# Kernel tuning notes

Hardware: AMD Instinct MI355X
Metric: run time of the kernel (lower is better)

Reference implementation:

```python
import jax, jax.numpy as jnp
import numpy as np

N, DIM, DK, DV = 8192, 1024, 128, 128


def setup_inputs() -> dict:
    key = jax.random.key(0)
    ks = jax.random.split(key, 5)
    # Match equinox Linear init scale roughly (uniform(-1/sqrt(in), 1/sqrt(in)))
    lim = 1.0 / np.sqrt(DIM)
    return {
        "x": jax.random.normal(ks[0], (N, DIM), dtype=jnp.float32),
        "Wqk": jax.random.uniform(ks[1], (DK, DIM), jnp.float32, -lim, lim),
        "bqk": jax.random.uniform(ks[2], (DK,), jnp.float32, -lim, lim),
        "Wv": jax.random.uniform(ks[3], (DV, DIM), jnp.float32, -lim, lim),
        "bv": jax.random.uniform(ks[4], (DV,), jnp.float32, -lim, lim),
    }


def reference(x, Wqk, bqk, Wv, bv):
    # shared QK projection: q == k == x @ Wqk^T + bqk  -> [n, dk]
    qk = jnp.einsum("nd,kd->nk", x, Wqk) + bqk
    v = jnp.einsum("nd,vd->nv", x, Wv) + bv  # [n, dv]
    # full n x n score matrix (no 1/sqrt(dk) scaling in the original)
    score = jnp.einsum("ik,jk->ij", qk, qk)  # [n, n]
    score = jax.nn.softmax(score, axis=-1)
    return jnp.einsum("ij,jv->iv", score, v)  # [n, dv]
```

## Files before the change

kernel.cpp:

```cpp
#include <hip/hip_runtime.h>
#include <math.h>

#define NROWS 8192
#define DIMX  1024
#define DKV   128
#define KSPLIT 4
#define KEYS_PER_SPLIT (NROWS / KSPLIT)
#define BN 64
#define QK_SCALE 1.2011224087864498f
#define M_FIX 96.0f

typedef __attribute__((ext_vector_type(8))) short bf16x8;
typedef __attribute__((ext_vector_type(4))) short s16x4;
typedef __attribute__((ext_vector_type(4))) float f32x4;

static __device__ __forceinline__ short f2bf(float f) {
    union { float f; unsigned u; } v; v.f = f;
    unsigned r = v.u + 0x7fff + ((v.u >> 16) & 1);
    return (short)(r >> 16);
}

__global__ __launch_bounds__(256) void wcvt_kernel(
    const float* __restrict__ Wqk, const float* __restrict__ bqk,
    const float* __restrict__ Wv,  const float* __restrict__ bv,
    short* __restrict__ wb, float* __restrict__ bb)
{
    const int idx = blockIdx.x * 1024 + threadIdx.x * 4;
    const bool isqk = idx < DKV * DIMX;
    const float* src = isqk ? (Wqk + idx) : (Wv + (idx - DKV * DIMX));
    const float sc = isqk ? QK_SCALE : 1.0f;
    const float4 f = *(const float4*)src;
    s16x4 o;
    o.x = f2bf(f.x * sc); o.y = f2bf(f.y * sc);
    o.z = f2bf(f.z * sc); o.w = f2bf(f.w * sc);
    *(s16x4*)&wb[idx] = o;
    if (blockIdx.x == 0) {
        const int t = threadIdx.x;
        bb[t] = (t < DKV) ? bqk[t] * QK_SCALE : bv[t - DKV];
    }
}

__global__ __launch_bounds__(256) void proj_kernel(
    const float* __restrict__ x, const short* __restrict__ wb,
    const float* __restrict__ bb, short* __restrict__ qkb, short* __restrict__ vtb)
{
    __shared__ __align__(16) short xb[32 * 1024];

    const int tid  = threadIdx.x;
    const int lane = tid & 63;
    const int wave = tid >> 6;
    const int l15  = lane & 15;
    const int quad = lane >> 4;
    const int mat  = blockIdx.y;
    const int rbase = blockIdx.x * 32;
    const int wr = wave >> 1, wc = wave & 1;
    const short* wsrc = wb + (size_t)mat * DKV * DIMX;

    #pragma unroll 8
    for (int i = 0; i < 32; ++i) {
        const float4 f = *(const float4*)(x + (size_t)(rbase + i) * DIMX + tid * 4);
        s16x4 o;
        o.x = f2bf(f.x); o.y = f2bf(f.y); o.z = f2bf(f.z); o.w = f2bf(f.w);
        *(s16x4*)&xb[i * 1024 + ((tid * 4) ^ ((i & 7) << 3))] = o;
    }
    __syncthreads();

    f32x4 acc[4];
    for (int i = 0; i < 4; ++i) acc[i] = (f32x4)0.0f;

    const int arow = wr * 16 + l15;
    const int aswz = (arow & 7) << 3;
    const short* arowp = &xb[arow * 1024];

    const short* wcol[4];
    for (int nt = 0; nt < 4; ++nt)
        wcol[nt] = wsrc + (size_t)(wc * 64 + nt * 16 + l15) * DIMX + quad * 8;

    bf16x8 bA[4], bB[4];
    for (int nt = 0; nt < 4; ++nt) bA[nt] = *(const bf16x8*)(wcol[nt]);

    for (int kk = 0; kk < 32; kk += 2) {
        for (int nt = 0; nt < 4; ++nt)
            bB[nt] = *(const bf16x8*)(wcol[nt] + (kk + 1) * 32);
        const bf16x8 a0 = *(const bf16x8*)&arowp[(kk * 32 + quad * 8) ^ aswz];
        for (int nt = 0; nt < 4; ++nt)
            acc[nt] = __builtin_amdgcn_mfma_f32_16x16x32_bf16(a0, bA[nt], acc[nt], 0, 0, 0);
        if (kk + 2 < 32)
            for (int nt = 0; nt < 4; ++nt)
                bA[nt] = *(const bf16x8*)(wcol[nt] + (kk + 2) * 32);
        const bf16x8 a1 = *(const bf16x8*)&arowp[((kk + 1) * 32 + quad * 8) ^ aswz];
        for (int nt = 0; nt < 4; ++nt)
            acc[nt] = __builtin_amdgcn_mfma_f32_16x16x32_bf16(a1, bB[nt], acc[nt], 0, 0, 0);
    }

    const int rw = rbase + wr * 16 + quad * 4;
    for (int nt = 0; nt < 4; ++nt) {
        const int col = wc * 64 + nt * 16 + l15;
        const float bias = bb[mat * DKV + col];
        if (mat == 0) {
            for (int r = 0; r < 4; ++r)
                qkb[(size_t)(rw + r) * DKV + col] = f2bf(acc[nt][r] + bias);
        } else {
            s16x4 o;
            o.x = f2bf(acc[nt][0] + bias); o.y = f2bf(acc[nt][1] + bias);
            o.z = f2bf(acc[nt][2] + bias); o.w = f2bf(acc[nt][3] + bias);
            *(s16x4*)&vtb[(size_t)col * NROWS + rw] = o;
        }
    }
}

__global__ __launch_bounds__(256, 2) void flash_kernel(
    const short* __restrict__ qkb, const short* __restrict__ vtb,
    float* __restrict__ opart, float* __restrict__ lpart)
{
    __shared__ __align__(16) short kt[2][64 * 128];
    __shared__ __align__(16) short pb[4][32 * 64];

    const int tid  = threadIdx.x;
    const int lane = tid & 63;
    const int wave = tid >> 6;
    const int l15  = lane & 15;
    const int quad = lane >> 4;
    const int rg   = wave >> 1;
    const int kh   = wave & 1;
    const int rbase = blockIdx.x * 64 + rg * 32;
    const int ks = blockIdx.y;

    unsigned koff[4];
    for (int i = 0; i < 4; ++i) {
        const int krow = wave * 16 + i * 4 + quad;
        koff[i] = (unsigned)krow * 256u
                + (((unsigned)l15 * 16u) ^ (((unsigned)krow & 7u) << 4));
    }

#define FL_ISSUE(buf, j0) do { \
        const char* kb_ = (const char*)qkb + (size_t)(j0) * (DKV * 2); \
        for (int i = 0; i < 4; ++i) \
            __builtin_amdgcn_global_load_lds( \
                (const __attribute__((address_space(1))) void*)(kb_ + koff[i]), \
                (__attribute__((address_space(3))) void*)((char*)&kt[buf][0] + (wave * 4 + i) * 1024), \
                16, 0, 0); \
    } while (0)

    const short* vpb = vtb + (size_t)l15 * NROWS + kh * 32 + quad * 8;
#define LOADV(dst, j0) do { \
        for (int nt_ = 0; nt_ < 8; ++nt_) \
            dst[nt_] = *(const bf16x8*)(vpb + (size_t)nt_ * (16 * NROWS) + (j0)); \
    } while (0)

    bf16x8 qf[2][4];
    #pragma unroll 2
    for (int h = 0; h < 2; ++h) {
        const short* qrow = qkb + (size_t)(rbase + h * 16 + l15) * DKV;
        for (int k = 0; k < 4; ++k)
            qf[h][k] = *(const bf16x8*)(qrow + k * 32 + quad * 8);
    }

    bf16x8 ones;
    for (int j = 0; j < 8; ++j) ones[j] = (short)0x3F80;

    f32x4 oacc[2][8];
    #pragma unroll 2
    for (int h = 0; h < 2; ++h)
        for (int i = 0; i < 8; ++i) oacc[h][i] = (f32x4)0.0f;
    f32x4 lsum[2] = {(f32x4)0.0f, (f32x4)0.0f};

    short* pw = &pb[wave][0];

    const int krow0 = kh * 32 + 2 * l15;
    const int swk0  = ((krow0 & 7) << 3);
    const int pxw = (quad & 1) << 6;
    const int pxr = (l15 & 4) << 4;

#define TILE(CUR, NXT, VC, VN, j0, more) do { \
        if (more) { FL_ISSUE(NXT, (j0) + BN); LOADV(VN, (j0) + BN); } \
        f32x4 s[2][2]; \
        __builtin_amdgcn_s_setprio(1); \
        for (int ntl = 0; ntl < 2; ++ntl) { \
            f32x4 a0 = (f32x4)0.0f, a1 = (f32x4)0.0f; \
            const int rowb = (krow0 + ntl) * 128; \
            const int swk  = swk0 + ntl * 8; \
            for (int k_ = 0; k_ < 4; ++k_) { \
                const bf16x8 b = *(const bf16x8*) \
                    &kt[CUR][rowb + ((k_ * 32 + quad * 8) ^ swk)]; \
                a0 = __builtin_amdgcn_mfma_f32_16x16x32_bf16(qf[0][k_], b, a0, 0, 0, 0); \
                a1 = __builtin_amdgcn_mfma_f32_16x16x32_bf16(qf[1][k_], b, a1, 0, 0, 0); \
            } \
            s[0][ntl] = a0; s[1][ntl] = a1; \
        } \
        __builtin_amdgcn_s_setprio(0); \
        for (int h = 0; h < 2; ++h) \
            for (int ntl = 0; ntl < 2; ++ntl) \
                for (int r = 0; r < 4; ++r) \
                    s[h][ntl][r] = __builtin_amdgcn_exp2f(s[h][ntl][r] - M_FIX); \
        for (int h = 0; h < 2; ++h) \
            for (int r = 0; r < 4; ++r) { \
                const int row = h * 16 + quad * 4 + r; \
                unsigned pk; \
                asm("v_cvt_pk_bf16_f32 %0, %1, %2" : "=v"(pk) : "v"(s[h][0][r]), "v"(s[h][1][r])); \
                *(unsigned*)((char*)pw + row * 128 + ((l15 * 4) ^ pxw)) = pk; \
            } \
        __builtin_amdgcn_s_setprio(1); \
        { \
            const bf16x8 a0 = *(const bf16x8*)((char*)pw + l15 * 128 + ((quad * 16) ^ pxr)); \
            const bf16x8 a1 = *(const bf16x8*)((char*)pw + (16 + l15) * 128 + ((quad * 16) ^ pxr)); \
            lsum[0] = __builtin_amdgcn_mfma_f32_16x16x32_bf16(a0, ones, lsum[0], 0, 0, 0); \
            lsum[1] = __builtin_amdgcn_mfma_f32_16x16x32_bf16(a1, ones, lsum[1], 0, 0, 0); \
            for (int nt_ = 0; nt_ < 8; ++nt_) { \
                oacc[0][nt_] = __builtin_amdgcn_mfma_f32_16x16x32_bf16(a0, VC[nt_], oacc[0][nt_], 0, 0, 0); \
                oacc[1][nt_] = __builtin_amdgcn_mfma_f32_16x16x32_bf16(a1, VC[nt_], oacc[1][nt_], 0, 0, 0); \
            } \
        } \
        __builtin_amdgcn_s_setprio(0); \
        __syncthreads();    \
    } while (0)

    const int j_begin = ks * KEYS_PER_SPLIT;
    const int j_end   = j_begin + KEYS_PER_SPLIT;

    bf16x8 vfA[8], vfB[8];
    FL_ISSUE(0, j_begin);
    LOADV(vfA, j_begin);
    __syncthreads();

    for (int j0 = j_begin; j0 < j_end; j0 += 2 * BN) {
        TILE(0, 1, vfA, vfB, j0, true);
        TILE(1, 0, vfB, vfA, j0 + BN, (j0 + 2 * BN) < j_end);
    }

    float* obuf = (float*)&kt[0][0] + rg * 32 * 128;
    float* lbuf = (float*)&pb[0][0];
    if (kh == 1) {
        #pragma unroll 2
        for (int h = 0; h < 2; ++h) {
            for (int nt = 0; nt < 8; ++nt)
                for (int r = 0; r < 4; ++r)
                    obuf[(h * 16 + quad * 4 + r) * 128 + nt * 16 + l15] = oacc[h][nt][r];
            if (l15 == 0)
                for (int r = 0; r < 4; ++r)
                    lbuf[rg * 32 + h * 16 + quad * 4 + r] = lsum[h][r];
        }
    }
    __syncthreads();
    if (kh == 0) {
        #pragma unroll 2
        for (int h = 0; h < 2; ++h) {
            const int rw = rbase + h * 16 + quad * 4;
            for (int nt = 0; nt < 8; ++nt) {
                const int col = nt * 16 + l15;
                for (int r = 0; r < 4; ++r)
                    opart[((size_t)ks * NROWS + rw + r) * DKV + col] =
                        oacc[h][nt][r] + obuf[(h * 16 + quad * 4 + r) * 128 + col];
            }
            if (l15 == 0)
                for (int r = 0; r < 4; ++r)
                    lpart[ks * NROWS + rw + r] =
                        lsum[h][r] + lbuf[rg * 32 + h * 16 + quad * 4 + r];
        }
    }
#undef FL_ISSUE
#undef LOADV
#undef TILE
}

__global__ __launch_bounds__(256) void combine_kernel(
    const float* __restrict__ opart, const float* __restrict__ lpart,
    float* __restrict__ out)
{
    const int idx = blockIdx.x * 256 + threadIdx.x;
    const int row = idx >> 7;
    float L = 0.f, acc = 0.f;
    for (int s = 0; s < KSPLIT; ++s) {
        L   += lpart[s * NROWS + row];
        acc += opart[(size_t)s * NROWS * DKV + idx];
    }
    out[idx] = acc / L;
}

extern "C" void kernel_launch(void* const* d_in, const int* in_sizes, int n_in,
                              void* d_out, int out_size, void* d_ws, size_t ws_size,
                              hipStream_t stream) {
    const float* x   = (const float*)d_in[0];
    const float* Wqk = (const float*)d_in[1];
    const float* bqk = (const float*)d_in[2];
    const float* Wv  = (const float*)d_in[3];
    const float* bv  = (const float*)d_in[4];
    float* out = (float*)d_out;

    char* ws = (char*)d_ws;
    short* qkb   = (short*)ws;
    short* vtb   = (short*)(ws + (2u << 20));
    short* wb    = (short*)(ws + (4u << 20));
    float* bb    = (float*)(ws + (4u << 20) + (512u << 10));
    float* opart = (float*)(ws + (5u << 20));
    float* lpart = (float*)(ws + (21u << 20));

    wcvt_kernel<<<dim3(256), 256, 0, stream>>>(Wqk, bqk, Wv, bv, wb, bb);
    proj_kernel<<<dim3(256, 2), 256, 0, stream>>>(x, wb, bb, qkb, vtb);
    flash_kernel<<<dim3(NROWS / 64, KSPLIT), 256, 0, stream>>>(qkb, vtb, opart, lpart);
    combine_kernel<<<dim3(NROWS * DKV / 256), 256, 0, stream>>>(opart, lpart, out);
}
```

Measured before the change: 191.0 us.

## Keep P in registers via transposed QK MFMA and stage V through LDS

The score MFMA now takes K as the A operand and Q as B, so its output is transposed and can be packed straight into the A operand of the PV MFMA. This removes the per-tile round trip of P through LDS. K rows are permuted at load time so the register layout lines up. V tiles are now prefetched into double-buffered, swizzled LDS with async global_load_lds instead of direct register loads, which frees VGPRs. The cost is more LDS traffic for V reads and a more complex row permutation that must stay correct.

```diff
diff --git a/kernel.cpp b/kernel.cpp
--- a/kernel.cpp
+++ b/kernel.cpp
@@ -13,6 +13,7 @@
 typedef __attribute__((ext_vector_type(8))) short bf16x8;
 typedef __attribute__((ext_vector_type(4))) short s16x4;
 typedef __attribute__((ext_vector_type(4))) float f32x4;
+typedef __attribute__((ext_vector_type(4))) unsigned u32x4;
 
 static __device__ __forceinline__ short f2bf(float f) {
     union { float f; unsigned u; } v; v.f = f;
@@ -114,7 +115,7 @@
     float* __restrict__ opart, float* __restrict__ lpart)
 {
     __shared__ __align__(16) short kt[2][64 * 128];
-    __shared__ __align__(16) short pb[4][32 * 64];
+    __shared__ __align__(16) short vt[2][128 * 64];
 
     const int tid  = threadIdx.x;
     const int lane = tid & 63;
@@ -125,27 +126,33 @@
     const int kh   = wave & 1;
     const int rbase = blockIdx.x * 64 + rg * 32;
     const int ks = blockIdx.y;
-
-    unsigned koff[4];
+    const int swzr = (l15 & 7) << 3;
+
+    unsigned koff[4], voff[4];
     for (int i = 0; i < 4; ++i) {
         const int krow = wave * 16 + i * 4 + quad;
-        koff[i] = (unsigned)krow * 256u
+        const int s = krow & 7;
+        const int srow = (krow & ~7) | (((s & 1) << 2) | (s >> 1));
+        koff[i] = (unsigned)srow * 256u
                 + (((unsigned)l15 * 16u) ^ (((unsigned)krow & 7u) << 4));
+        const int vrow = wave * 32 + i * 8 + (lane >> 3);
+        voff[i] = (unsigned)vrow * (unsigned)(NROWS * 2)
+                + ((((unsigned)lane & 7u) * 16u) ^ (((unsigned)vrow & 7u) << 4));
     }
 
 #define FL_ISSUE(buf, j0) do { \
         const char* kb_ = (const char*)qkb + (size_t)(j0) * (DKV * 2); \
+        const char* vb_ = (const char*)vtb + (size_t)(j0) * 2; \
         for (int i = 0; i < 4; ++i) \
             __builtin_amdgcn_global_load_lds( \
                 (const __attribute__((address_space(1))) void*)(kb_ + koff[i]), \
                 (__attribute__((address_space(3))) void*)((char*)&kt[buf][0] + (wave * 4 + i) * 1024), \
                 16, 0, 0); \
-    } while (0)
-
-    const short* vpb = vtb + (size_t)l15 * NROWS + kh * 32 + quad * 8;
-#define LOADV(dst, j0) do { \
-        for (int nt_ = 0; nt_ < 8; ++nt_) \
-            dst[nt_] = *(const bf16x8*)(vpb + (size_t)nt_ * (16 * NROWS) + (j0)); \
+        for (int i = 0; i < 4; ++i) \
+            __builtin_amdgcn_global_load_lds( \
+                (const __attribute__((address_space(1))) void*)(vb_ + voff[i]), \
+                (__attribute__((address_space(3))) void*)((char*)&vt[buf][0] + (wave * 4 + i) * 1024), \
+                16, 0, 0); \
     } while (0)
 
     bf16x8 qf[2][4];
@@ -165,15 +172,11 @@
         for (int i = 0; i < 8; ++i) oacc[h][i] = (f32x4)0.0f;
     f32x4 lsum[2] = {(f32x4)0.0f, (f32x4)0.0f};
 
-    short* pw = &pb[wave][0];
-
     const int krow0 = kh * 32 + 2 * l15;
     const int swk0  = ((krow0 & 7) << 3);
-    const int pxw = (quad & 1) << 6;
-    const int pxr = (l15 & 4) << 4;
-
-#define TILE(CUR, NXT, VC, VN, j0, more) do { \
-        if (more) { FL_ISSUE(NXT, (j0) + BN); LOADV(VN, (j0) + BN); } \
+
+#define TILE(CUR, NXT, j0, more) do { \
+        if (more) FL_ISSUE(NXT, (j0) + BN); \
         f32x4 s[2][2]; \
         __builtin_amdgcn_s_setprio(1); \
         for (int ntl = 0; ntl < 2; ++ntl) { \
@@ -181,10 +184,10 @@
             const int rowb = (krow0 + ntl) * 128; \
             const int swk  = swk0 + ntl * 8; \
             for (int k_ = 0; k_ < 4; ++k_) { \
-                const bf16x8 b = *(const bf16x8*) \
+                const bf16x8 kb = *(const bf16x8*) \
                     &kt[CUR][rowb + ((k_ * 32 + quad * 8) ^ swk)]; \
-                a0 = __builtin_amdgcn_mfma_f32_16x16x32_bf16(qf[0][k_], b, a0, 0, 0, 0); \
-                a1 = __builtin_amdgcn_mfma_f32_16x16x32_bf16(qf[1][k_], b, a1, 0, 0, 0); \
+                a0 = __builtin_amdgcn_mfma_f32_16x16x32_bf16(kb, qf[0][k_], a0, 0, 0, 0); \
+                a1 = __builtin_amdgcn_mfma_f32_16x16x32_bf16(kb, qf[1][k_], a1, 0, 0, 0); \
             } \
             s[0][ntl] = a0; s[1][ntl] = a1; \
         } \
@@ -193,23 +196,23 @@
             for (int ntl = 0; ntl < 2; ++ntl) \
                 for (int r = 0; r < 4; ++r) \
                     s[h][ntl][r] = __builtin_amdgcn_exp2f(s[h][ntl][r] - M_FIX); \
-        for (int h = 0; h < 2; ++h) \
-            for (int r = 0; r < 4; ++r) { \
-                const int row = h * 16 + quad * 4 + r; \
-                unsigned pk; \
-                asm("v_cvt_pk_bf16_f32 %0, %1, %2" : "=v"(pk) : "v"(s[h][0][r]), "v"(s[h][1][r])); \
-                *(unsigned*)((char*)pw + row * 128 + ((l15 * 4) ^ pxw)) = pk; \
-            } \
+        bf16x8 pa[2]; \
+        for (int h = 0; h < 2; ++h) { \
+            u32x4 t; \
+            asm("v_cvt_pk_bf16_f32 %0, %1, %2" : "=v"(t.x) : "v"(s[h][0][0]), "v"(s[h][0][1])); \
+            asm("v_cvt_pk_bf16_f32 %0, %1, %2" : "=v"(t.y) : "v"(s[h][0][2]), "v"(s[h][0][3])); \
+            asm("v_cvt_pk_bf16_f32 %0, %1, %2" : "=v"(t.z) : "v"(s[h][1][0]), "v"(s[h][1][1])); \
+            asm("v_cvt_pk_bf16_f32 %0, %1, %2" : "=v"(t.w) : "v"(s[h][1][2]), "v"(s[h][1][3])); \
+            pa[h] = *(bf16x8*)&t; \
+        } \
         __builtin_amdgcn_s_setprio(1); \
-        { \
-            const bf16x8 a0 = *(const bf16x8*)((char*)pw + l15 * 128 + ((quad * 16) ^ pxr)); \
-            const bf16x8 a1 = *(const bf16x8*)((char*)pw + (16 + l15) * 128 + ((quad * 16) ^ pxr)); \
-            lsum[0] = __builtin_amdgcn_mfma_f32_16x16x32_bf16(a0, ones, lsum[0], 0, 0, 0); \
-            lsum[1] = __builtin_amdgcn_mfma_f32_16x16x32_bf16(a1, ones, lsum[1], 0, 0, 0); \
-            for (int nt_ = 0; nt_ < 8; ++nt_) { \
-                oacc[0][nt_] = __builtin_amdgcn_mfma_f32_16x16x32_bf16(a0, VC[nt_], oacc[0][nt_], 0, 0, 0); \
-                oacc[1][nt_] = __builtin_amdgcn_mfma_f32_16x16x32_bf16(a1, VC[nt_], oacc[1][nt_], 0, 0, 0); \
-            } \
+        lsum[0] = __builtin_amdgcn_mfma_f32_16x16x32_bf16(pa[0], ones, lsum[0], 0, 0, 0); \
+        lsum[1] = __builtin_amdgcn_mfma_f32_16x16x32_bf16(pa[1], ones, lsum[1], 0, 0, 0); \
+        for (int nt_ = 0; nt_ < 8; ++nt_) { \
+            const bf16x8 vb = *(const bf16x8*) \
+                &vt[CUR][(nt_ * 16 + l15) * 64 + ((kh * 32 + quad * 8) ^ swzr)]; \
+            oacc[0][nt_] = __builtin_amdgcn_mfma_f32_16x16x32_bf16(pa[0], vb, oacc[0][nt_], 0, 0, 0); \
+            oacc[1][nt_] = __builtin_amdgcn_mfma_f32_16x16x32_bf16(pa[1], vb, oacc[1][nt_], 0, 0, 0); \
         } \
         __builtin_amdgcn_s_setprio(0); \
         __syncthreads();    \
@@ -218,18 +221,16 @@
     const int j_begin = ks * KEYS_PER_SPLIT;
     const int j_end   = j_begin + KEYS_PER_SPLIT;
 
-    bf16x8 vfA[8], vfB[8];
     FL_ISSUE(0, j_begin);
-    LOADV(vfA, j_begin);
     __syncthreads();
 
     for (int j0 = j_begin; j0 < j_end; j0 += 2 * BN) {
-        TILE(0, 1, vfA, vfB, j0, true);
-        TILE(1, 0, vfB, vfA, j0 + BN, (j0 + 2 * BN) < j_end);
+        TILE(0, 1, j0, true);
+        TILE(1, 0, j0 + BN, (j0 + 2 * BN) < j_end);
     }
 
     float* obuf = (float*)&kt[0][0] + rg * 32 * 128;
-    float* lbuf = (float*)&pb[0][0];
+    float* lbuf = (float*)&vt[0][0];
     if (kh == 1) {
         #pragma unroll 2
         for (int h = 0; h < 2; ++h) {
@@ -259,7 +260,6 @@
         }
     }
 #undef FL_ISSUE
-#undef LOADV
 #undef TILE
 }
 
```

Result: faster. 156.2 us (-18.2%).
